# Optimization experiments

Hardware: AMD Instinct MI355X
Metric: run time of the kernel (lower is better)

The kernel has to match this reference:

```python
import jax, jax.numpy as jnp
import numpy as np

B, S, H, V = 4, 512, 256, 32000


def setup_inputs() -> dict:
    key = jax.random.key(0)
    ks = jax.random.split(key, 6)
    s = 0.02
    x = jax.random.randint(ks[0], (B, S), 0, V)
    emb = jax.random.normal(ks[1], (V, H), dtype=jnp.float32) * s
    W_ih = jax.random.normal(ks[2], (3 * H, H), dtype=jnp.float32) * s
    W_hh = jax.random.normal(ks[3], (3 * H, H), dtype=jnp.float32) * s
    b_ih = jnp.zeros((3 * H,), jnp.float32)
    b_hh = jnp.zeros((3 * H,), jnp.float32)
    W_out = jax.random.normal(ks[4], (V, H), dtype=jnp.float32) * s
    b_out = jnp.zeros((V,), jnp.float32)
    return dict(x=x, emb=emb, W_ih=W_ih, W_hh=W_hh, b_ih=b_ih, b_hh=b_hh,
                W_out=W_out, b_out=b_out)


def gru_sequence(embedded, W_ih, W_hh, b_ih, b_hh):
    # embedded: [B, S, H]; precompute all input projections once: [B, S, 3H]
    xp = jnp.einsum('bsh,gh->bsg', embedded, W_ih) + b_ih
    Hdim = W_hh.shape[1]
    h0 = jnp.zeros((embedded.shape[0], Hdim), embedded.dtype)

    def step(h, xt):  # xt: [B, 3H]
        hp = h @ W_hh.T + b_hh  # [B, 3H]
        xr, xz, xn = jnp.split(xt, 3, axis=-1)
        hr, hz, hn = jnp.split(hp, 3, axis=-1)
        r = jax.nn.sigmoid(xr + hr)
        z = jax.nn.sigmoid(xz + hz)
        n = jnp.tanh(xn + r * hn)
        h_new = (1.0 - z) * n + z * h
        return h_new, h_new

    _, hs = jax.lax.scan(step, h0, jnp.swapaxes(xp, 0, 1))  # [S, B, H]
    return jnp.swapaxes(hs, 0, 1)  # [B, S, H]


def reference(x, emb, W_ih, W_hh, b_ih, b_hh, W_out, b_out):
    embedded = emb[x]                                   # [B, S, H]
    rnn_out = gru_sequence(embedded, W_ih, W_hh, b_ih, b_hh)
    logits = jnp.einsum('bsh,vh->bsv', rnn_out, W_out) + b_out  # [B, S, V]
    # symbolic constraint: if prev token == 0, tokens >= 3 are invalid (t > 0)
    prev_zero = (x[:, :-1] == 0)                        # [B, S-1]
    prev_zero = jnp.pad(prev_zero, ((0, 0), (1, 0)))    # t=0 never masked
    vocab_ge3 = jnp.arange(logits.shape[-1]) >= 3       # [V]
    invalid = prev_zero[:, :, None] & vocab_ge3[None, None, :]
    return jnp.where(invalid, -jnp.inf, logits)
```

## Files before the change

kernel.cpp:

```cpp
#include <hip/hip_runtime.h>
#include <hip/hip_bf16.h>

typedef __attribute__((ext_vector_type(8))) short bf16x8;
typedef __attribute__((ext_vector_type(4))) float f32x4;
typedef __attribute__((ext_vector_type(2))) float f32x2;
typedef __attribute__((ext_vector_type(4))) unsigned short u16x4;

#define HB 256
#define G3 768
#define SQ 512
#define NBATCH 4
#define NV 32000

__device__ __forceinline__ unsigned short f2bf(float f) {
    unsigned int u = __float_as_uint(f);
    u = u + 0x7FFFu + ((u >> 16) & 1u);
    return (unsigned short)(u >> 16);
}

__global__ void k_prep(const float* __restrict__ W_ih, const float* __restrict__ W_hh,
                       float* __restrict__ w_ihT, unsigned short* __restrict__ wfrag) {
    int stride = gridDim.x * blockDim.x;
    int tid = blockIdx.x * blockDim.x + threadIdx.x;
    for (int e = tid; e < G3 * HB; e += stride) {
        int k = e / G3, g = e - k * G3;
        w_ihT[e] = W_ih[g * HB + k];
    }
    for (int e = tid; e < G3 * HB; e += stride) {
        int i = e & 7, l = (e >> 3) & 63, c = (e >> 9) & 7, rt = (e >> 12) & 1;
        int q = e >> 13;
        int t = q % 3, w = q / 3;
        int row = t * 256 + 32 * w + 16 * rt + (l & 15);
        int kk = 32 * c + 8 * (l >> 4) + i;
        wfrag[e] = f2bf(W_hh[row * HB + kk]);
    }
}

__global__ __launch_bounds__(256) void k_embed_xp(
        const int* __restrict__ x, const float* __restrict__ emb,
        const float* __restrict__ w_ihT, const float* __restrict__ b_ih,
        const float* __restrict__ b_hh, float* __restrict__ xp) {
    __shared__ float e[8][HB];
    int tid = threadIdx.x;
    int tok0 = blockIdx.x * 8;
    {
        int s = tid >> 5, k0 = (tid & 31) * 8;
        long idx = x[tok0 + s];
        const float* src = emb + idx * (long)HB + k0;
        f32x4 a = *(const f32x4*)src, bq = *(const f32x4*)(src + 4);
        *(f32x4*)&e[s][k0] = a;
        *(f32x4*)&e[s][k0 + 4] = bq;
    }
    __syncthreads();
    #pragma unroll
    for (int it = 0; it < 3; ++it) {
        int gg = tid + it * 256;
        float acc[8] = {0.f, 0.f, 0.f, 0.f, 0.f, 0.f, 0.f, 0.f};
        for (int k = 0; k < HB; k += 4) {
            float w0 = w_ihT[(k + 0) * G3 + gg];
            float w1 = w_ihT[(k + 1) * G3 + gg];
            float w2 = w_ihT[(k + 2) * G3 + gg];
            float w3 = w_ihT[(k + 3) * G3 + gg];
            #pragma unroll
            for (int s = 0; s < 8; ++s) {
                f32x4 ev = *(const f32x4*)&e[s][k];
                acc[s] += w0 * ev.x + w1 * ev.y + w2 * ev.z + w3 * ev.w;
            }
        }
        float bias = b_ih[gg] + (gg < 512 ? b_hh[gg] : 0.f);
        #pragma unroll
        for (int s = 0; s < 8; ++s)
            xp[(size_t)(tok0 + s) * G3 + gg] = acc[s] + bias;
    }
}

__global__ __attribute__((amdgpu_waves_per_eu(2, 2))) __launch_bounds__(512)
void k_gru(const float* __restrict__ xp, const unsigned short* __restrict__ wfrag,
           const float* __restrict__ b_hh, unsigned short* __restrict__ rnn,
           const float* __restrict__ W_out, unsigned short* __restrict__ woutbf,
           int do_wout) {
    __shared__ unsigned short hbf[2][NBATCH][HB];

    int tid = threadIdx.x;

    if (blockIdx.x != 0) {
        if (!do_wout) return;
        int bt = (blockIdx.x - 1) * 512 + tid;
        const f32x4* src = (const f32x4*)W_out;
        u16x4* dst = (u16x4*)woutbf;
        for (int qd = bt; qd < NV * HB / 4; qd += 64 * 512) {
            f32x4 v = src[qd];
            u16x4 o;
            o[0] = f2bf(v.x); o[1] = f2bf(v.y); o[2] = f2bf(v.z); o[3] = f2bf(v.w);
            dst[qd] = o;
        }
        return;
    }

    int w = tid >> 6, l = tid & 63;
    int c15 = l & 15, hi = l >> 4;
    int b4 = c15 & 3;
    int q = c15 >> 2;
    int rt = q & 1, jh = q >> 1;
    int swz = (b4 & 1) << 6;

    bf16x8 Arz[2][2][8];
    bf16x8 An[2][8];
    #pragma unroll
    for (int g = 0; g < 2; ++g)
        #pragma unroll
        for (int r2 = 0; r2 < 2; ++r2)
            #pragma unroll
            for (int c = 0; c < 8; ++c) {
                Arz[g][r2][c] = ((const bf16x8*)wfrag)[(((w * 3 + g) * 2 + r2) * 8 + c) * 64 + l];
                asm volatile("" : "+a"(Arz[g][r2][c]));
            }
    #pragma unroll
    for (int r2 = 0; r2 < 2; ++r2)
        #pragma unroll
        for (int c = 0; c < 8; ++c) {
            An[r2][c] = ((const bf16x8*)wfrag)[(((w * 3 + 2) * 2 + r2) * 8 + c) * 64 + l];
            asm volatile("" : "+v"(An[r2][c]));
        }

    for (int k = tid; k < 2 * NBATCH * HB; k += 512) ((unsigned short*)hbf)[k] = 0;

    int row0 = 32 * w + 16 * rt + 4 * hi + 2 * jh;
    f32x2 bn = *(const f32x2*)&b_hh[512 + row0];
    float H0 = 0.f, H1 = 0.f;
    const f32x4 zz = {0.f, 0.f, 0.f, 0.f};

    const float* xpb = xp + (size_t)b4 * SQ * G3 + row0;
    unsigned short* rnb = rnn + (size_t)b4 * SQ * HB + row0;
    const char* rdb = (const char*)hbf + b4 * 512;
    char* wrb = (char*)hbf + b4 * 512 + ((row0 * 2) ^ swz);
    __syncthreads();

    for (int t = 0; t < SQ; ++t) {
        int cur = (t & 1) << 11, nxt = cur ^ 2048;

        f32x2 xr = *(const f32x2*)(xpb);
        f32x2 xz = *(const f32x2*)(xpb + 256);
        f32x2 xn = *(const f32x2*)(xpb + 512);

        f32x4 a0 = zz, a1 = zz, a2 = zz, a3 = zz, a4 = zz, a5 = zz;
        #pragma unroll
        for (int c = 0; c < 8; ++c) {
            bf16x8 Bf = *(const bf16x8*)(rdb + cur + ((64 * c + 16 * hi) ^ swz));
            asm("v_mfma_f32_16x16x32_bf16 %0, %1, %2, %0" : "+v"(a0) : "a"(Arz[0][0][c]), "v"(Bf));
            asm("v_mfma_f32_16x16x32_bf16 %0, %1, %2, %0" : "+v"(a1) : "a"(Arz[0][1][c]), "v"(Bf));
            asm("v_mfma_f32_16x16x32_bf16 %0, %1, %2, %0" : "+v"(a2) : "a"(Arz[1][0][c]), "v"(Bf));
            asm("v_mfma_f32_16x16x32_bf16 %0, %1, %2, %0" : "+v"(a3) : "a"(Arz[1][1][c]), "v"(Bf));
            a4 = __builtin_amdgcn_mfma_f32_16x16x32_bf16(An[0][c], Bf, a4, 0, 0, 0);
            a5 = __builtin_amdgcn_mfma_f32_16x16x32_bf16(An[1][c], Bf, a5, 0, 0, 0);
        }
        __builtin_amdgcn_sched_barrier(0);
        asm volatile("s_nop 7\n\ts_nop 7");
        __builtin_amdgcn_sched_barrier(0);

        bool brt = rt != 0, bjh = jh != 0;
        f32x4 vr = brt ? a1 : a0;
        f32x4 vz = brt ? a3 : a2;
        f32x4 vn = brt ? a5 : a4;
        float sr0 = bjh ? vr.z : vr.x, sr1 = bjh ? vr.w : vr.y;
        float sz0 = bjh ? vz.z : vz.x, sz1 = bjh ? vz.w : vz.y;
        float sn0 = bjh ? vn.z : vn.x, sn1 = bjh ? vn.w : vn.y;

        float r0 = __builtin_amdgcn_rcpf(1.f + __expf(-(xr.x + sr0)));
        float z0 = __builtin_amdgcn_rcpf(1.f + __expf(-(xz.x + sz0)));
        float n0 = 1.f - 2.f * __builtin_amdgcn_rcpf(__expf(2.f * (xn.x + r0 * (sn0 + bn.x))) + 1.f);
        float h0 = (1.f - z0) * n0 + z0 * H0;
        H0 = h0;
        float r1 = __builtin_amdgcn_rcpf(1.f + __expf(-(xr.y + sr1)));
        float z1 = __builtin_amdgcn_rcpf(1.f + __expf(-(xz.y + sz1)));
        float n1 = 1.f - 2.f * __builtin_amdgcn_rcpf(__expf(2.f * (xn.y + r1 * (sn1 + bn.y))) + 1.f);
        float h1 = (1.f - z1) * n1 + z1 * H1;
        H1 = h1;

        unsigned int pk;
        asm("v_cvt_pk_bf16_f32 %0, %1, %2" : "=v"(pk) : "v"(h0), "v"(h1));
        *(unsigned int*)(wrb + nxt) = pk;
        *(unsigned int*)rnb = pk;

        asm volatile("s_waitcnt lgkmcnt(0)" ::: "memory");
        __builtin_amdgcn_sched_barrier(0);
        __builtin_amdgcn_s_barrier();

        xpb += G3;
        rnb += HB;
    }
}

template <int CONV>
__global__ __launch_bounds__(512) void k_logits(
        const unsigned short* __restrict__ rnn, const unsigned short* __restrict__ woutbf,
        const float* __restrict__ woutf, const float* __restrict__ b_out,
        const int* __restrict__ x, float* __restrict__ out) {
    int fid = blockIdx.x;
    int g = (fid & 7) * 250 + (fid >> 3);
    int bx = g >> 3;
    int by = g & 7;

    int tid = threadIdx.x;
    int wv = tid >> 6, l = tid & 63;
    int wm = wv >> 1, wn = wv & 1;
    int c15 = l & 15, hi = l >> 4;
    int m0 = by * 256 + wm * 64;
    int n0 = bx * 128 + wn * 64;

    const f32x4 zz = {0.f, 0.f, 0.f, 0.f};
    f32x4 acc[4][4];
    #pragma unroll
    for (int i = 0; i < 4; ++i)
        #pragma unroll
        for (int j = 0; j < 4; ++j) acc[i][j] = zz;

    #pragma unroll
    for (int c = 0; c < 8; ++c) {
        bf16x8 af[4], bfr[4];
        #pragma unroll
        for (int rt = 0; rt < 4; ++rt)
            af[rt] = *(const bf16x8*)(rnn + (size_t)(m0 + rt * 16 + c15) * HB + 32 * c + 8 * hi);
        #pragma unroll
        for (int ct = 0; ct < 4; ++ct) {
            if (CONV) {
                const float* s = woutf + (size_t)(n0 + ct * 16 + c15) * HB + 32 * c + 8 * hi;
                f32x4 lo = *(const f32x4*)s, hi4 = *(const f32x4*)(s + 4);
                bf16x8 bb;
                #pragma unroll
                for (int qq = 0; qq < 4; ++qq) bb[qq] = (short)f2bf(lo[qq]);
                #pragma unroll
                for (int qq = 0; qq < 4; ++qq) bb[4 + qq] = (short)f2bf(hi4[qq]);
                bfr[ct] = bb;
            } else {
                bfr[ct] = *(const bf16x8*)(woutbf + (size_t)(n0 + ct * 16 + c15) * HB + 32 * c + 8 * hi);
            }
        }
        #pragma unroll
        for (int rt = 0; rt < 4; ++rt)
            #pragma unroll
            for (int ct = 0; ct < 4; ++ct)
                acc[rt][ct] = __builtin_amdgcn_mfma_f32_16x16x32_bf16(af[rt], bfr[ct], acc[rt][ct], 0, 0, 0);
    }

    float bo[4];
    #pragma unroll
    for (int ct = 0; ct < 4; ++ct) bo[ct] = b_out[n0 + ct * 16 + c15];

    const float NEGINF = -__builtin_inff();
    #pragma unroll
    for (int rt = 0; rt < 4; ++rt) {
        #pragma unroll
        for (int j = 0; j < 4; ++j) {
            int m = m0 + rt * 16 + 4 * hi + j;
            int tt = m & (SQ - 1);
            bool bad = (tt > 0) && (x[m - 1] == 0);
            float* orow = out + (size_t)m * NV;
            #pragma unroll
            for (int ct = 0; ct < 4; ++ct) {
                int v = n0 + ct * 16 + c15;
                float val = acc[rt][ct][j] + bo[ct];
                if (bad && v >= 3) val = NEGINF;
                __builtin_nontemporal_store(val, &orow[v]);
            }
        }
    }
}

extern "C" void kernel_launch(void* const* d_in, const int* in_sizes, int n_in,
                              void* d_out, int out_size, void* d_ws, size_t ws_size,
                              hipStream_t stream) {
    const int*   x     = (const int*)d_in[0];
    const float* emb   = (const float*)d_in[1];
    const float* W_ih  = (const float*)d_in[2];
    const float* W_hh  = (const float*)d_in[3];
    const float* b_ih  = (const float*)d_in[4];
    const float* b_hh  = (const float*)d_in[5];
    const float* W_out = (const float*)d_in[6];
    const float* b_out = (const float*)d_in[7];
    float* out = (float*)d_out;

    char* ws = (char*)d_ws;
    float*          xp     = (float*)(ws);
    float*          w_ihT  = (float*)(ws + 6291456);
    unsigned short* wfrag  = (unsigned short*)(ws + 7077888);
    unsigned short* rnn    = (unsigned short*)(ws + 7471104);
    unsigned short* woutbf = (unsigned short*)(ws + 8519680);
    int use_woutbf = (ws_size >= (size_t)24903680) ? 1 : 0;

    k_prep<<<512, 256, 0, stream>>>(W_ih, W_hh, w_ihT, wfrag);
    k_embed_xp<<<256, 256, 0, stream>>>(x, emb, w_ihT, b_ih, b_hh, xp);
    k_gru<<<65, 512, 0, stream>>>(xp, wfrag, b_hh, rnn, W_out, woutbf, use_woutbf);
    if (use_woutbf)
        k_logits<0><<<2000, 512, 0, stream>>>(rnn, woutbf, nullptr, b_out, x, out);
    else
        k_logits<1><<<2000, 512, 0, stream>>>(rnn, nullptr, W_out, b_out, x, out);
}
```

Measured before the change: 773.1 us.

## Fuse logits GEMM into GRU kernel with flag-based producer-consumer overlap

Merges the recurrent GRU and the output projection into one persistent launch. Block 0 runs the serial recurrence and publishes a step counter every 64 steps. The other 255 blocks first convert W_out to bf16 and sync on a global counter. They then compute 128-row logits tiles as soon as the matching time range is ready, so most of the projection and output writes overlap the latency-bound recurrence. The trade-offs are memory-bandwidth contention with the critical GRU block, spin-wait polling, a dropped nontemporal store hint, and a slower fallback path if the workspace lacks room for the flags.

```diff
diff --git a/kernel.cpp b/kernel.cpp
--- a/kernel.cpp
+++ b/kernel.cpp
@@ -11,6 +11,7 @@
 #define SQ 512
 #define NBATCH 4
 #define NV 32000
+#define NPAIR 2000
 
 __device__ __forceinline__ unsigned short f2bf(float f) {
     unsigned int u = __float_as_uint(f);
@@ -19,7 +20,9 @@
 }
 
 __global__ void k_prep(const float* __restrict__ W_ih, const float* __restrict__ W_hh,
-                       float* __restrict__ w_ihT, unsigned short* __restrict__ wfrag) {
+                       float* __restrict__ w_ihT, unsigned short* __restrict__ wfrag,
+                       int* flags) {
+    if (flags && blockIdx.x == 0 && threadIdx.x == 0) { flags[0] = 0; flags[1] = 0; }
     int stride = gridDim.x * blockDim.x;
     int tid = blockIdx.x * blockDim.x + threadIdx.x;
     for (int e = tid; e < G3 * HB; e += stride) {
@@ -74,25 +77,102 @@
     }
 }
 
+__device__ __forceinline__ void logits_tile(
+        const unsigned short* __restrict__ rnn, const unsigned short* __restrict__ woutbf,
+        const float* __restrict__ b_out, const int* __restrict__ x,
+        float* __restrict__ out, int bx, int by, int ltid) {
+    int wv = ltid >> 6, l = ltid & 63;
+    int wm = wv >> 1, wn = wv & 1;
+    int c15 = l & 15, hi = l >> 4;
+    int m0 = by * 128 + wm * 64;
+    int n0 = bx * 128 + wn * 64;
+
+    const f32x4 zz = {0.f, 0.f, 0.f, 0.f};
+    f32x4 acc[4][4];
+    #pragma unroll
+    for (int i = 0; i < 4; ++i)
+        #pragma unroll
+        for (int j = 0; j < 4; ++j) acc[i][j] = zz;
+
+    #pragma unroll
+    for (int c = 0; c < 8; ++c) {
+        bf16x8 af[4], bfr[4];
+        #pragma unroll
+        for (int rt = 0; rt < 4; ++rt)
+            af[rt] = *(const bf16x8*)(rnn + (size_t)(m0 + rt * 16 + c15) * HB + 32 * c + 8 * hi);
+        #pragma unroll
+        for (int ct = 0; ct < 4; ++ct)
+            bfr[ct] = *(const bf16x8*)(woutbf + (size_t)(n0 + ct * 16 + c15) * HB + 32 * c + 8 * hi);
+        #pragma unroll
+        for (int rt = 0; rt < 4; ++rt)
+            #pragma unroll
+            for (int ct = 0; ct < 4; ++ct)
+                acc[rt][ct] = __builtin_amdgcn_mfma_f32_16x16x32_bf16(af[rt], bfr[ct], acc[rt][ct], 0, 0, 0);
+    }
+
+    float bo[4];
+    #pragma unroll
+    for (int ct = 0; ct < 4; ++ct) bo[ct] = b_out[n0 + ct * 16 + c15];
+
+    const float NEGINF = -__builtin_inff();
+    #pragma unroll
+    for (int rt = 0; rt < 4; ++rt) {
+        #pragma unroll
+        for (int j = 0; j < 4; ++j) {
+            int m = m0 + rt * 16 + 4 * hi + j;
+            int tt = m & (SQ - 1);
+            bool bad = (tt > 0) && (x[m - 1] == 0);
+            float* orow = out + (size_t)m * NV;
+            #pragma unroll
+            for (int ct = 0; ct < 4; ++ct) {
+                int v = n0 + ct * 16 + c15;
+                float val = acc[rt][ct][j] + bo[ct];
+                if (bad && v >= 3) val = NEGINF;
+                orow[v] = val;
+            }
+        }
+    }
+}
+
+template <int OVL>
 __global__ __attribute__((amdgpu_waves_per_eu(2, 2))) __launch_bounds__(512)
-void k_gru(const float* __restrict__ xp, const unsigned short* __restrict__ wfrag,
-           const float* __restrict__ b_hh, unsigned short* __restrict__ rnn,
-           const float* __restrict__ W_out, unsigned short* __restrict__ woutbf,
-           int do_wout) {
+void k_main(const float* __restrict__ xp, const unsigned short* __restrict__ wfrag,
+            const float* __restrict__ b_hh, unsigned short* __restrict__ rnn,
+            const float* __restrict__ W_out, unsigned short* __restrict__ woutbf,
+            const float* __restrict__ b_out, const int* __restrict__ x,
+            float* __restrict__ out, int* flags) {
     __shared__ unsigned short hbf[2][NBATCH][HB];
-
     int tid = threadIdx.x;
 
     if (blockIdx.x != 0) {
-        if (!do_wout) return;
-        int bt = (blockIdx.x - 1) * 512 + tid;
-        const f32x4* src = (const f32x4*)W_out;
-        u16x4* dst = (u16x4*)woutbf;
-        for (int qd = bt; qd < NV * HB / 4; qd += 64 * 512) {
-            f32x4 v = src[qd];
-            u16x4 o;
-            o[0] = f2bf(v.x); o[1] = f2bf(v.y); o[2] = f2bf(v.z); o[3] = f2bf(v.w);
-            dst[qd] = o;
+        if (!OVL) return;
+        {
+            const f32x4* src = (const f32x4*)W_out;
+            u16x4* dst = (u16x4*)woutbf;
+            int start = (int)(blockIdx.x - 1) * 512 + tid;
+            for (int qd = start; qd < NV * HB / 4; qd += 255 * 512) {
+                f32x4 v = src[qd];
+                u16x4 o;
+                o[0] = f2bf(v.x); o[1] = f2bf(v.y); o[2] = f2bf(v.z); o[3] = f2bf(v.w);
+                dst[qd] = o;
+            }
+        }
+        __syncthreads();
+        if (tid == 0)
+            __hip_atomic_fetch_add(&flags[1], 1, __ATOMIC_ACQ_REL, __HIP_MEMORY_SCOPE_AGENT);
+        while (__hip_atomic_load(&flags[1], __ATOMIC_RELAXED, __HIP_MEMORY_SCOPE_AGENT) < 255)
+            __builtin_amdgcn_s_sleep(8);
+        __builtin_amdgcn_fence(__ATOMIC_ACQUIRE, "agent");
+
+        int half = tid >> 8, ltid = tid & 255;
+        for (int p = (int)(blockIdx.x - 1); p < NPAIR; p += 255) {
+            int tile = 2 * p + half;
+            int by = tile / 250, bx = tile - by * 250;
+            int need = ((by & 3) + 1) * 128;
+            while (__hip_atomic_load(&flags[0], __ATOMIC_RELAXED, __HIP_MEMORY_SCOPE_AGENT) < need)
+                __builtin_amdgcn_s_sleep(8);
+            __builtin_amdgcn_fence(__ATOMIC_ACQUIRE, "agent");
+            logits_tile(rnn, woutbf, b_out, x, out, bx, by, ltid);
         }
         return;
     }
@@ -182,30 +262,33 @@
         *(unsigned int*)(wrb + nxt) = pk;
         *(unsigned int*)rnb = pk;
 
-        asm volatile("s_waitcnt lgkmcnt(0)" ::: "memory");
+        if (OVL && ((t & 63) == 63))
+            asm volatile("s_waitcnt vmcnt(0) lgkmcnt(0)" ::: "memory");
+        else
+            asm volatile("s_waitcnt lgkmcnt(0)" ::: "memory");
         __builtin_amdgcn_sched_barrier(0);
         __builtin_amdgcn_s_barrier();
+        if (OVL && ((t & 63) == 63) && tid == 0)
+            __hip_atomic_store(&flags[0], t + 1, __ATOMIC_RELEASE, __HIP_MEMORY_SCOPE_AGENT);
 
         xpb += G3;
         rnb += HB;
     }
 }
 
-template <int CONV>
-__global__ __launch_bounds__(512) void k_logits(
-        const unsigned short* __restrict__ rnn, const unsigned short* __restrict__ woutbf,
-        const float* __restrict__ woutf, const float* __restrict__ b_out,
-        const int* __restrict__ x, float* __restrict__ out) {
+__global__ __launch_bounds__(256) void k_logits_fb(
+        const unsigned short* __restrict__ rnn, const float* __restrict__ woutf,
+        const float* __restrict__ b_out, const int* __restrict__ x,
+        float* __restrict__ out) {
     int fid = blockIdx.x;
-    int g = (fid & 7) * 250 + (fid >> 3);
-    int bx = g >> 3;
-    int by = g & 7;
+    int g = (fid & 7) * 500 + (fid >> 3);
+    int bx = g >> 4, by = g & 15;
 
     int tid = threadIdx.x;
     int wv = tid >> 6, l = tid & 63;
     int wm = wv >> 1, wn = wv & 1;
     int c15 = l & 15, hi = l >> 4;
-    int m0 = by * 256 + wm * 64;
+    int m0 = by * 128 + wm * 64;
     int n0 = bx * 128 + wn * 64;
 
     const f32x4 zz = {0.f, 0.f, 0.f, 0.f};
@@ -223,18 +306,14 @@
             af[rt] = *(const bf16x8*)(rnn + (size_t)(m0 + rt * 16 + c15) * HB + 32 * c + 8 * hi);
         #pragma unroll
         for (int ct = 0; ct < 4; ++ct) {
-            if (CONV) {
-                const float* s = woutf + (size_t)(n0 + ct * 16 + c15) * HB + 32 * c + 8 * hi;
-                f32x4 lo = *(const f32x4*)s, hi4 = *(const f32x4*)(s + 4);
-                bf16x8 bb;
-                #pragma unroll
-                for (int qq = 0; qq < 4; ++qq) bb[qq] = (short)f2bf(lo[qq]);
-                #pragma unroll
-                for (int qq = 0; qq < 4; ++qq) bb[4 + qq] = (short)f2bf(hi4[qq]);
-                bfr[ct] = bb;
-            } else {
-                bfr[ct] = *(const bf16x8*)(woutbf + (size_t)(n0 + ct * 16 + c15) * HB + 32 * c + 8 * hi);
-            }
+            const float* s = woutf + (size_t)(n0 + ct * 16 + c15) * HB + 32 * c + 8 * hi;
+            f32x4 lo = *(const f32x4*)s, hi4 = *(const f32x4*)(s + 4);
+            bf16x8 bb;
+            #pragma unroll
+            for (int qq = 0; qq < 4; ++qq) bb[qq] = (short)f2bf(lo[qq]);
+            #pragma unroll
+            for (int qq = 0; qq < 4; ++qq) bb[4 + qq] = (short)f2bf(hi4[qq]);
+            bfr[ct] = bb;
         }
         #pragma unroll
         for (int rt = 0; rt < 4; ++rt)
@@ -261,7 +340,7 @@
                 int v = n0 + ct * 16 + c15;
                 float val = acc[rt][ct][j] + bo[ct];
                 if (bad && v >= 3) val = NEGINF;
-                __builtin_nontemporal_store(val, &orow[v]);
+                orow[v] = val;
             }
         }
     }
@@ -286,13 +365,17 @@
     unsigned short* wfrag  = (unsigned short*)(ws + 7077888);
     unsigned short* rnn    = (unsigned short*)(ws + 7471104);
     unsigned short* woutbf = (unsigned short*)(ws + 8519680);
-    int use_woutbf = (ws_size >= (size_t)24903680) ? 1 : 0;
-
-    k_prep<<<512, 256, 0, stream>>>(W_ih, W_hh, w_ihT, wfrag);
+    int*            flags  = (int*)(ws + 24903680);
+    int ovl = (ws_size >= (size_t)(24903680 + 64)) ? 1 : 0;
+
+    k_prep<<<512, 256, 0, stream>>>(W_ih, W_hh, w_ihT, wfrag, ovl ? flags : nullptr);
     k_embed_xp<<<256, 256, 0, stream>>>(x, emb, w_ihT, b_ih, b_hh, xp);
-    k_gru<<<65, 512, 0, stream>>>(xp, wfrag, b_hh, rnn, W_out, woutbf, use_woutbf);
-    if (use_woutbf)
-        k_logits<0><<<2000, 512, 0, stream>>>(rnn, woutbf, nullptr, b_out, x, out);
-    else
-        k_logits<1><<<2000, 512, 0, stream>>>(rnn, nullptr, W_out, b_out, x, out);
-}
+    if (ovl) {
+        k_main<1><<<256, 512, 0, stream>>>(xp, wfrag, b_hh, rnn, W_out, woutbf,
+                                           b_out, x, out, flags);
+    } else {
+        k_main<0><<<1, 512, 0, stream>>>(xp, wfrag, b_hh, rnn, W_out, woutbf,
+                                         b_out, x, out, nullptr);
+        k_logits_fb<<<4000, 256, 0, stream>>>(rnn, W_out, b_out, x, out);
+    }
+}
```

Measured after the change: 849.7 us. 1.1x slower.
